# Performance work log

Measured on AMD Instinct MI355X. Metric: run time of the kernel, lower is better.

Reference implementation:

```python
import jax, jax.numpy as jnp
import numpy as np

B, S, D, H = 2, 2048, 1024, 16
HD = D // H


def setup_inputs() -> dict:
    key = jax.random.key(0)
    ks = jax.random.split(key, 7)
    q = jax.random.normal(ks[0], (B, S, D), jnp.float32)
    k = jax.random.normal(ks[1], (B, S, D), jnp.float32)
    v = jax.random.normal(ks[2], (B, S, D), jnp.float32)
    attention_mask = jnp.ones((B, S), jnp.int32)  # padding mask, 1 = keep
    bound = float(np.sqrt(6.0 / (D + D)))  # xavier_uniform for square Linear
    Wq = jax.random.uniform(ks[3], (D, D), jnp.float32, -bound, bound)
    Wk = jax.random.uniform(ks[4], (D, D), jnp.float32, -bound, bound)
    Wv = jax.random.uniform(ks[5], (D, D), jnp.float32, -bound, bound)
    Wo = jax.random.uniform(ks[6], (D, D), jnp.float32, -bound, bound)
    return {"q": q, "k": k, "v": v, "attention_mask": attention_mask,
            "Wq": Wq, "Wk": Wk, "Wv": Wv, "Wo": Wo}


def reference(q, k, v, attention_mask, Wq, Wk, Wv, Wo):
    # nn.Linear (bias=False): y = x @ W.T ; then split heads [B,H,S,HD]
    def heads(x, W):
        return (x @ W.T).reshape(B, S, H, HD).transpose(0, 2, 1, 3)

    qh, kh, vh = heads(q, Wq), heads(k, Wk), heads(v, Wv)
    scale = 1.0 / jnp.sqrt(jnp.float32(HD))
    # causal additive mask (0 on/below diagonal, -inf above); adding before the
    # scale matches the original since -inf * scale == -inf
    causal = jnp.where(jnp.tril(jnp.ones((S, S), dtype=bool)), 0.0, -jnp.inf)
    attn = (jnp.einsum('bhld,bhsd->bhls', qh, kh) + causal) * scale  # [B,H,L,S]
    pad = attention_mask[:, None, None, :]  # [B,1,1,S] padding mask
    attn = jnp.where(pad == 0, -jnp.inf, attn)
    attn = jax.nn.softmax(attn, axis=-1)
    out = jnp.einsum('bhls,bhsd->bhld', attn, vh)
    out = out.transpose(0, 2, 1, 3).reshape(B, S, D)
    return out @ Wo.T
```

## Files before the change

kernel.cpp:

```cpp
#include <hip/hip_runtime.h>
#include <hip/hip_bf16.h>
#include <stdint.h>

#define DEV_INLINE __device__ __forceinline__

typedef unsigned short u16;
typedef __attribute__((ext_vector_type(8))) __bf16 bf16x8;
typedef __attribute__((ext_vector_type(4))) float f32x4;

constexpr int Bc = 2, Sc = 2048, Dc = 1024, Hc = 16, HDc = 64;
constexpr int Kdim = 1024;
constexpr size_t SEG4M = 4194304;
constexpr size_t SEG1M = 1048576;

DEV_INLINE u16 f32_to_bf16(float f) {
    unsigned int u = __builtin_bit_cast(unsigned int, f);
    unsigned int r = (u + 0x7fffu + ((u >> 16) & 1u)) >> 16;
    return (u16)r;
}

DEV_INLINE uint32_t cvtpk_bf16(float lo, float hi) {
    uint32_t r;
    asm("v_cvt_pk_bf16_f32 %0, %1, %2" : "=v"(r) : "v"(lo), "v"(hi));
    return r;
}

DEV_INLINE f32x4 mfma16(bf16x8 a, bf16x8 b, f32x4 c) {
    return __builtin_amdgcn_mfma_f32_16x16x32_bf16(a, b, c, 0, 0, 0);
}

DEV_INLINE void gload_lds16(const u16* g, u16* lds) {
    __builtin_amdgcn_global_load_lds(
        (const __attribute__((address_space(1))) void*)g,
        (__attribute__((address_space(3))) void*)lds,
        16, 0, 0);
}

__global__ __launch_bounds__(256) void cvt_all_kernel(
        const float* __restrict__ q, const float* __restrict__ k,
        const float* __restrict__ v, const float* __restrict__ wq,
        const float* __restrict__ wk, const float* __restrict__ wv,
        const float* __restrict__ wo, u16* __restrict__ dst) {
    int b = blockIdx.x;
    const float* src; size_t doff; int lb;
    if (b < 2048)      { src = q;  lb = b;        doff = 0; }
    else if (b < 4096) { src = k;  lb = b - 2048; doff = SEG4M; }
    else if (b < 6144) { src = v;  lb = b - 4096; doff = 2 * SEG4M; }
    else if (b < 6656) { src = wq; lb = b - 6144; doff = 3 * SEG4M; }
    else if (b < 7168) { src = wk; lb = b - 6656; doff = 3 * SEG4M + SEG1M; }
    else if (b < 7680) { src = wv; lb = b - 7168; doff = 3 * SEG4M + 2 * SEG1M; }
    else               { src = wo; lb = b - 7680; doff = 3 * SEG4M + 3 * SEG1M; }
    size_t i = ((size_t)lb * 256 + threadIdx.x) * 8;
    float4 a = *reinterpret_cast<const float4*>(src + i);
    float4 c = *reinterpret_cast<const float4*>(src + i + 4);
    union { u16 u[8]; uint4 v4; } o;
    o.u[0] = f32_to_bf16(a.x); o.u[1] = f32_to_bf16(a.y);
    o.u[2] = f32_to_bf16(a.z); o.u[3] = f32_to_bf16(a.w);
    o.u[4] = f32_to_bf16(c.x); o.u[5] = f32_to_bf16(c.y);
    o.u[6] = f32_to_bf16(c.z); o.u[7] = f32_to_bf16(c.w);
    *reinterpret_cast<uint4*>(dst + doff + i) = o.v4;
}

__global__ __launch_bounds__(256, 3) void gemm_qkv_kernel(
        const u16* __restrict__ Xb, const u16* __restrict__ Wb,
        u16* __restrict__ Ob) {
    __shared__ u16 Al[128 * 64];
    __shared__ u16 Bl[128 * 64];
    const int tid = threadIdx.x;
    const int l = tid & 63, w = tid >> 6;
    const int wm = w >> 1, wn = w & 1;
    const int l15 = l & 15, lg = l >> 4;
    const int lr = l >> 3, lc = (l & 7) * 8;

    int bid = blockIdx.x;
    int wid = (bid & 7) * 96 + (bid >> 3);
    int mt = wid / 24, nt = wid % 24;
    int seg = nt >> 3, ntl = nt & 7;

    const u16* A = Xb + (size_t)seg * SEG4M + (size_t)mt * 128 * Kdim;
    const u16* W = Wb + (size_t)seg * SEG1M + (size_t)ntl * 128 * Kdim;

    f32x4 acc[4][4] = {};

    for (int kt = 0; kt < 16; ++kt) {
        const int kb = kt * 64;
#pragma unroll
        for (int i = 0; i < 4; ++i) {
            int j = w * 4 + i;
            gload_lds16(A + (size_t)(j * 8 + lr) * Kdim + kb + lc, &Al[j * 512]);
            gload_lds16(W + (size_t)(j * 8 + lr) * Kdim + kb + lc, &Bl[j * 512]);
        }
        asm volatile("s_waitcnt vmcnt(0)" ::: "memory");
        __syncthreads();
#pragma unroll
        for (int kk = 0; kk < 2; ++kk) {
            bf16x8 af[4], bfr[4];
#pragma unroll
            for (int mi = 0; mi < 4; ++mi)
                af[mi] = *reinterpret_cast<const bf16x8*>(&Al[(wm * 64 + mi * 16 + l15) * 64 + kk * 32 + lg * 8]);
#pragma unroll
            for (int ni = 0; ni < 4; ++ni)
                bfr[ni] = *reinterpret_cast<const bf16x8*>(&Bl[(wn * 64 + ni * 16 + l15) * 64 + kk * 32 + lg * 8]);
#pragma unroll
            for (int mi = 0; mi < 4; ++mi)
#pragma unroll
                for (int ni = 0; ni < 4; ++ni)
                    acc[mi][ni] = mfma16(af[mi], bfr[ni], acc[mi][ni]);
        }
        __syncthreads();
    }

    const int row0 = mt * 128 + wm * 64;
    const int col0 = ntl * 128 + wn * 64;

    if (seg == 2) {
        u16* outT = Ob + 2 * SEG4M;
#pragma unroll
        for (int mi = 0; mi < 4; ++mi) {
            int m0 = row0 + mi * 16 + lg * 4;
            int b = m0 >> 11, s0 = m0 & 2047;
#pragma unroll
            for (int ni = 0; ni < 4; ++ni) {
                int n = col0 + ni * 16 + l15;
                int h = n >> 6, d = n & 63;
                int bh = b * Hc + h;
                uint2 pk;
                pk.x = ((uint32_t)f32_to_bf16(acc[mi][ni][1]) << 16) | f32_to_bf16(acc[mi][ni][0]);
                pk.y = ((uint32_t)f32_to_bf16(acc[mi][ni][3]) << 16) | f32_to_bf16(acc[mi][ni][2]);
                *reinterpret_cast<uint2*>(outT + ((size_t)bh * 64 + d) * Sc + s0) = pk;
            }
        }
    } else {
        const float scale = (seg == 0) ? 0.18033688f : 1.0f;
        u16* out = Ob + (size_t)seg * SEG4M;
#pragma unroll
        for (int mi = 0; mi < 4; ++mi)
#pragma unroll
            for (int r = 0; r < 4; ++r) {
                int m = row0 + mi * 16 + lg * 4 + r;
                int b = m >> 11, s = m & 2047;
#pragma unroll
                for (int ni = 0; ni < 4; ++ni) {
                    int n = col0 + ni * 16 + l15;
                    int h = n >> 6, d = n & 63;
                    out[(((size_t)b * Hc + h) * Sc + s) * HDc + d] =
                        f32_to_bf16(acc[mi][ni][r] * scale);
                }
            }
    }
}

__global__ __launch_bounds__(256, 3) void gemm_out_kernel(
        const u16* __restrict__ A0, const u16* __restrict__ W0,
        float* __restrict__ outf) {
    __shared__ u16 Al[128 * 64];
    __shared__ u16 Bl[64 * 64];
    const int tid = threadIdx.x;
    const int l = tid & 63, w = tid >> 6;
    const int l15 = l & 15, lg = l >> 4;
    const int lr = l >> 3, lc = (l & 7) * 8;

    int bid = blockIdx.x;
    int wid = (bid & 7) * 64 + (bid >> 3);
    int mt = wid >> 4, nt = wid & 15;

    const u16* A = A0 + (size_t)mt * 128 * Kdim;
    const u16* W = W0 + (size_t)nt * 64 * Kdim;

    f32x4 acc[2][4] = {};

    for (int kt = 0; kt < 16; ++kt) {
        const int kb = kt * 64;
#pragma unroll
        for (int i = 0; i < 4; ++i) {
            int j = w * 4 + i;
            gload_lds16(A + (size_t)(j * 8 + lr) * Kdim + kb + lc, &Al[j * 512]);
        }
#pragma unroll
        for (int i = 0; i < 2; ++i) {
            int j = w * 2 + i;
            gload_lds16(W + (size_t)(j * 8 + lr) * Kdim + kb + lc, &Bl[j * 512]);
        }
        asm volatile("s_waitcnt vmcnt(0)" ::: "memory");
        __syncthreads();
#pragma unroll
        for (int kk = 0; kk < 2; ++kk) {
            bf16x8 af[2], bfr[4];
#pragma unroll
            for (int mi = 0; mi < 2; ++mi)
                af[mi] = *reinterpret_cast<const bf16x8*>(&Al[(w * 32 + mi * 16 + l15) * 64 + kk * 32 + lg * 8]);
#pragma unroll
            for (int ni = 0; ni < 4; ++ni)
                bfr[ni] = *reinterpret_cast<const bf16x8*>(&Bl[(ni * 16 + l15) * 64 + kk * 32 + lg * 8]);
#pragma unroll
            for (int mi = 0; mi < 2; ++mi)
#pragma unroll
                for (int ni = 0; ni < 4; ++ni)
                    acc[mi][ni] = mfma16(af[mi], bfr[ni], acc[mi][ni]);
        }
        __syncthreads();
    }

#pragma unroll
    for (int mi = 0; mi < 2; ++mi)
#pragma unroll
        for (int r = 0; r < 4; ++r) {
            int m = mt * 128 + w * 32 + mi * 16 + lg * 4 + r;
#pragma unroll
            for (int ni = 0; ni < 4; ++ni) {
                int n = nt * 64 + ni * 16 + l15;
                outf[(size_t)m * 1024 + n] = acc[mi][ni][r];
            }
        }
}

__global__ __launch_bounds__(512, 4) void flash_attn_kernel(
        const u16* __restrict__ Qh, const u16* __restrict__ Kh,
        const u16* __restrict__ Vt, u16* __restrict__ Ctx) {
    __shared__ u16 Ksh[64][72];
    __shared__ u16 Vsh[64][72];
    __shared__ u16 Psh[8][16][72];

    const int tid = threadIdx.x;
    const int l = tid & 63, w = tid >> 6;
    const int l15 = l & 15, lg = l >> 4;

    const int bid = blockIdx.x;
    const int bh = bid & 31;
    const int qt = 15 - (bid >> 5);
    const int b = bh >> 4, h = bh & 15;
    const int qr0 = qt * 128 + w * 16;

    const u16* qb = Qh + ((size_t)bh * Sc + qr0) * 64;
    bf16x8 aq[2];
#pragma unroll
    for (int kk = 0; kk < 2; ++kk)
        aq[kk] = *reinterpret_cast<const bf16x8*>(
            qb + (size_t)l15 * 64 + kk * 32 + lg * 8);

    f32x4 o[4] = {};
    float m_run = -1e30f, l_run = 0.f;

    const u16* kb0 = Kh + (size_t)bh * Sc * 64;
    const u16* vb0 = Vt + (size_t)bh * 64 * Sc;
    const int nkt = 2 * qt + 2;
    const int kt_max_w = qr0 >> 6;

    uint4 rk, rv;
    auto load_kv = [&](int kt) {
        int r = tid >> 3, cc = (tid & 7) * 8;
        rk = *reinterpret_cast<const uint4*>(kb0 + ((size_t)kt * 64 + r) * 64 + cc);
        rv = *reinterpret_cast<const uint4*>(vb0 + (size_t)r * Sc + kt * 64 + cc);
    };
    auto store_kv = [&]() {
        int r = tid >> 3, cc = (tid & 7) * 8;
        *reinterpret_cast<uint4*>(&Ksh[r][cc]) = rk;
        *reinterpret_cast<uint4*>(&Vsh[r][cc]) = rv;
    };

    load_kv(0);
    for (int kt = 0; kt < nkt; ++kt) {
        store_kv();
        __syncthreads();
        if (kt + 1 < nkt) load_kv(kt + 1);

        if (kt <= kt_max_w) {
            f32x4 sc[4] = {};
#pragma unroll
            for (int kk = 0; kk < 2; ++kk) {
                bf16x8 kf[4];
#pragma unroll
                for (int nk = 0; nk < 4; ++nk)
                    kf[nk] = *reinterpret_cast<const bf16x8*>(&Ksh[nk * 16 + l15][kk * 32 + lg * 8]);
                __builtin_amdgcn_s_setprio(1);
#pragma unroll
                for (int nk = 0; nk < 4; ++nk)
                    sc[nk] = mfma16(kf[nk], aq[kk], sc[nk]);
                __builtin_amdgcn_s_setprio(0);
            }

            if (kt == kt_max_w) {
                const int kb = kt * 64 + lg * 4;
                const int qg = qr0 + l15;
#pragma unroll
                for (int nk = 0; nk < 4; ++nk)
#pragma unroll
                    for (int r = 0; r < 4; ++r)
                        if (kb + nk * 16 + r > qg) sc[nk][r] = -1e30f;
            }

            float pmax = -1e30f;
#pragma unroll
            for (int nk = 0; nk < 4; ++nk)
#pragma unroll
                for (int r = 0; r < 4; ++r) pmax = fmaxf(pmax, sc[nk][r]);
            pmax = fmaxf(pmax, __shfl_xor(pmax, 16));
            pmax = fmaxf(pmax, __shfl_xor(pmax, 32));
            if (pmax > m_run + 11.5f) {
                float alpha = exp2f(m_run - pmax);
                l_run *= alpha;
#pragma unroll
                for (int nd = 0; nd < 4; ++nd)
#pragma unroll
                    for (int r = 0; r < 4; ++r) o[nd][r] *= alpha;
                m_run = pmax;
            }
            float ssum = 0.f;
#pragma unroll
            for (int nk = 0; nk < 4; ++nk)
#pragma unroll
                for (int r = 0; r < 4; ++r) {
                    float p = exp2f(sc[nk][r] - m_run);
                    sc[nk][r] = p;
                    ssum += p;
                }
            ssum += __shfl_xor(ssum, 16);
            ssum += __shfl_xor(ssum, 32);
            l_run += ssum;
#pragma unroll
            for (int nk = 0; nk < 4; ++nk) {
                uint2 pk;
                pk.x = cvtpk_bf16(sc[nk][0], sc[nk][1]);
                pk.y = cvtpk_bf16(sc[nk][2], sc[nk][3]);
                *reinterpret_cast<uint2*>(&Psh[w][l15][nk * 16 + lg * 4]) = pk;
            }
            asm volatile("s_waitcnt lgkmcnt(0)" ::: "memory");
            __builtin_amdgcn_sched_barrier(0);

#pragma unroll
            for (int kk = 0; kk < 2; ++kk) {
                bf16x8 vf[4];
#pragma unroll
                for (int nd = 0; nd < 4; ++nd)
                    vf[nd] = *reinterpret_cast<const bf16x8*>(&Vsh[nd * 16 + l15][kk * 32 + lg * 8]);
                bf16x8 pa = *reinterpret_cast<const bf16x8*>(&Psh[w][l15][kk * 32 + lg * 8]);
                __builtin_amdgcn_s_setprio(1);
#pragma unroll
                for (int nd = 0; nd < 4; ++nd)
                    o[nd] = mfma16(vf[nd], pa, o[nd]);
                __builtin_amdgcn_s_setprio(0);
            }
        }
        __syncthreads();
    }

    {
        float inv = 1.f / l_run;
        int srow = qr0 + l15;
        size_t base = ((size_t)b * Sc + srow) * Dc + h * 64;
#pragma unroll
        for (int nd = 0; nd < 4; ++nd) {
            uint2 pk;
            pk.x = cvtpk_bf16(o[nd][0] * inv, o[nd][1] * inv);
            pk.y = cvtpk_bf16(o[nd][2] * inv, o[nd][3] * inv);
            *reinterpret_cast<uint2*>(Ctx + base + nd * 16 + lg * 4) = pk;
        }
    }
}

extern "C" void kernel_launch(void* const* d_in, const int* in_sizes, int n_in,
                              void* d_out, int out_size, void* d_ws, size_t ws_size,
                              hipStream_t stream) {
    const float* q  = (const float*)d_in[0];
    const float* k  = (const float*)d_in[1];
    const float* v  = (const float*)d_in[2];
    const float* Wq = (const float*)d_in[4];
    const float* Wk = (const float*)d_in[5];
    const float* Wv = (const float*)d_in[6];
    const float* Wo = (const float*)d_in[7];

    u16* ws = (u16*)d_ws;
    u16* Xq  = ws;
    u16* Wqb = ws + 3 * SEG4M;
    u16* Wob = Wqb + 3 * SEG1M;
    u16* Qh  = ws + 4 * SEG4M;
    u16* Kh  = Qh + SEG4M;
    u16* Vtr = Kh + SEG4M;
    u16* Ctx = ws;

    cvt_all_kernel<<<8192, 256, 0, stream>>>(q, k, v, Wq, Wk, Wv, Wo, ws);

    gemm_qkv_kernel<<<768, 256, 0, stream>>>(Xq, Wqb, Qh);

    flash_attn_kernel<<<512, 512, 0, stream>>>(Qh, Kh, Vtr, Ctx);

    gemm_out_kernel<<<512, 256, 0, stream>>>(Ctx, Wob, (float*)d_out);
}
```

Measured before the change: 123.9 us.

## Switch flash attention to 32x32x16 MFMA with register-resident P fragments

The attention kernel now has 4 waves per block, each covering 32 query rows, and uses 32x32x16 bf16 MFMAs instead of 16x16x32. The softmax probabilities are packed to bf16 and rearranged between half-waves with cross-lane shuffles, so they no longer round-trip through LDS. This removes the P shared buffer and its waitcnt barrier and cuts the row reductions to one shuffle step. In exchange each thread holds more accumulator registers and does more K/V staging loads, and the block shrinks to 256 threads, which changes occupancy.

```diff
diff --git a/kernel.cpp b/kernel.cpp
--- a/kernel.cpp
+++ b/kernel.cpp
@@ -7,6 +7,7 @@
 typedef unsigned short u16;
 typedef __attribute__((ext_vector_type(8))) __bf16 bf16x8;
 typedef __attribute__((ext_vector_type(4))) float f32x4;
+typedef __attribute__((ext_vector_type(16))) float f32x16;
 
 constexpr int Bc = 2, Sc = 2048, Dc = 1024, Hc = 16, HDc = 64;
 constexpr int Kdim = 1024;
@@ -27,6 +28,9 @@
 
 DEV_INLINE f32x4 mfma16(bf16x8 a, bf16x8 b, f32x4 c) {
     return __builtin_amdgcn_mfma_f32_16x16x32_bf16(a, b, c, 0, 0, 0);
+}
+DEV_INLINE f32x16 mfma32(bf16x8 a, bf16x8 b, f32x16 c) {
+    return __builtin_amdgcn_mfma_f32_32x32x16_bf16(a, b, c, 0, 0, 0);
 }
 
 DEV_INLINE void gload_lds16(const u16* g, u16* lds) {
@@ -214,31 +218,31 @@
         }
 }
 
-__global__ __launch_bounds__(512, 4) void flash_attn_kernel(
+__global__ __launch_bounds__(256, 2) void flash_attn_kernel(
         const u16* __restrict__ Qh, const u16* __restrict__ Kh,
         const u16* __restrict__ Vt, u16* __restrict__ Ctx) {
     __shared__ u16 Ksh[64][72];
     __shared__ u16 Vsh[64][72];
-    __shared__ u16 Psh[8][16][72];
 
     const int tid = threadIdx.x;
     const int l = tid & 63, w = tid >> 6;
-    const int l15 = l & 15, lg = l >> 4;
+    const int l31 = l & 31;
+    const int h = l >> 5;
 
     const int bid = blockIdx.x;
     const int bh = bid & 31;
     const int qt = 15 - (bid >> 5);
-    const int b = bh >> 4, h = bh & 15;
-    const int qr0 = qt * 128 + w * 16;
-
-    const u16* qb = Qh + ((size_t)bh * Sc + qr0) * 64;
-    bf16x8 aq[2];
-#pragma unroll
-    for (int kk = 0; kk < 2; ++kk)
-        aq[kk] = *reinterpret_cast<const bf16x8*>(
-            qb + (size_t)l15 * 64 + kk * 32 + lg * 8);
-
-    f32x4 o[4] = {};
+    const int b = bh >> 4, hh = bh & 15;
+    const int qr0 = qt * 128 + w * 32;
+    const int q = qr0 + l31;
+
+    const u16* qb = Qh + ((size_t)bh * Sc + q) * 64;
+    bf16x8 aq[4];
+#pragma unroll
+    for (int s = 0; s < 4; ++s)
+        aq[s] = *reinterpret_cast<const bf16x8*>(qb + s * 16 + h * 8);
+
+    f32x16 o[2] = {};
     float m_run = -1e30f, l_run = 0.f;
 
     const u16* kb0 = Kh + (size_t)bh * Sc * 64;
@@ -252,92 +256,113 @@
         rk = *reinterpret_cast<const uint4*>(kb0 + ((size_t)kt * 64 + r) * 64 + cc);
         rv = *reinterpret_cast<const uint4*>(vb0 + (size_t)r * Sc + kt * 64 + cc);
     };
+    uint4 rk2, rv2;
+    auto load_kv2 = [&](int kt) {
+        int r = 32 + (tid >> 3), cc = (tid & 7) * 8;
+        rk2 = *reinterpret_cast<const uint4*>(kb0 + ((size_t)kt * 64 + r) * 64 + cc);
+        rv2 = *reinterpret_cast<const uint4*>(vb0 + (size_t)r * Sc + kt * 64 + cc);
+    };
     auto store_kv = [&]() {
         int r = tid >> 3, cc = (tid & 7) * 8;
         *reinterpret_cast<uint4*>(&Ksh[r][cc]) = rk;
         *reinterpret_cast<uint4*>(&Vsh[r][cc]) = rv;
+        *reinterpret_cast<uint4*>(&Ksh[32 + r][cc]) = rk2;
+        *reinterpret_cast<uint4*>(&Vsh[32 + r][cc]) = rv2;
     };
 
-    load_kv(0);
+    load_kv(0); load_kv2(0);
     for (int kt = 0; kt < nkt; ++kt) {
         store_kv();
         __syncthreads();
-        if (kt + 1 < nkt) load_kv(kt + 1);
+        if (kt + 1 < nkt) { load_kv(kt + 1); load_kv2(kt + 1); }
 
         if (kt <= kt_max_w) {
-            f32x4 sc[4] = {};
-#pragma unroll
-            for (int kk = 0; kk < 2; ++kk) {
-                bf16x8 kf[4];
-#pragma unroll
-                for (int nk = 0; nk < 4; ++nk)
-                    kf[nk] = *reinterpret_cast<const bf16x8*>(&Ksh[nk * 16 + l15][kk * 32 + lg * 8]);
+            f32x16 sc[2] = {};
+#pragma unroll
+            for (int s = 0; s < 4; ++s) {
+                bf16x8 kf0 = *reinterpret_cast<const bf16x8*>(&Ksh[l31][s * 16 + h * 8]);
+                bf16x8 kf1 = *reinterpret_cast<const bf16x8*>(&Ksh[32 + l31][s * 16 + h * 8]);
                 __builtin_amdgcn_s_setprio(1);
-#pragma unroll
-                for (int nk = 0; nk < 4; ++nk)
-                    sc[nk] = mfma16(kf[nk], aq[kk], sc[nk]);
+                sc[0] = mfma32(kf0, aq[s], sc[0]);
+                sc[1] = mfma32(kf1, aq[s], sc[1]);
                 __builtin_amdgcn_s_setprio(0);
             }
 
             if (kt == kt_max_w) {
-                const int kb = kt * 64 + lg * 4;
-                const int qg = qr0 + l15;
-#pragma unroll
-                for (int nk = 0; nk < 4; ++nk)
-#pragma unroll
-                    for (int r = 0; r < 4; ++r)
-                        if (kb + nk * 16 + r > qg) sc[nk][r] = -1e30f;
+#pragma unroll
+                for (int nk = 0; nk < 2; ++nk)
+#pragma unroll
+                    for (int r = 0; r < 16; ++r) {
+                        int kpos = kt * 64 + nk * 32 + (r & 3) + 8 * (r >> 2) + 4 * h;
+                        if (kpos > q) sc[nk][r] = -1e30f;
+                    }
             }
 
             float pmax = -1e30f;
 #pragma unroll
-            for (int nk = 0; nk < 4; ++nk)
-#pragma unroll
-                for (int r = 0; r < 4; ++r) pmax = fmaxf(pmax, sc[nk][r]);
-            pmax = fmaxf(pmax, __shfl_xor(pmax, 16));
+            for (int nk = 0; nk < 2; ++nk)
+#pragma unroll
+                for (int r = 0; r < 16; ++r) pmax = fmaxf(pmax, sc[nk][r]);
             pmax = fmaxf(pmax, __shfl_xor(pmax, 32));
             if (pmax > m_run + 11.5f) {
                 float alpha = exp2f(m_run - pmax);
                 l_run *= alpha;
 #pragma unroll
-                for (int nd = 0; nd < 4; ++nd)
-#pragma unroll
-                    for (int r = 0; r < 4; ++r) o[nd][r] *= alpha;
+                for (int nd = 0; nd < 2; ++nd)
+#pragma unroll
+                    for (int r = 0; r < 16; ++r) o[nd][r] *= alpha;
                 m_run = pmax;
             }
             float ssum = 0.f;
 #pragma unroll
-            for (int nk = 0; nk < 4; ++nk)
-#pragma unroll
-                for (int r = 0; r < 4; ++r) {
+            for (int nk = 0; nk < 2; ++nk)
+#pragma unroll
+                for (int r = 0; r < 16; ++r) {
                     float p = exp2f(sc[nk][r] - m_run);
                     sc[nk][r] = p;
                     ssum += p;
                 }
-            ssum += __shfl_xor(ssum, 16);
             ssum += __shfl_xor(ssum, 32);
             l_run += ssum;
-#pragma unroll
-            for (int nk = 0; nk < 4; ++nk) {
-                uint2 pk;
-                pk.x = cvtpk_bf16(sc[nk][0], sc[nk][1]);
-                pk.y = cvtpk_bf16(sc[nk][2], sc[nk][3]);
-                *reinterpret_cast<uint2*>(&Psh[w][l15][nk * 16 + lg * 4]) = pk;
-            }
-            asm volatile("s_waitcnt lgkmcnt(0)" ::: "memory");
-            __builtin_amdgcn_sched_barrier(0);
-
-#pragma unroll
-            for (int kk = 0; kk < 2; ++kk) {
-                bf16x8 vf[4];
-#pragma unroll
-                for (int nd = 0; nd < 4; ++nd)
-                    vf[nd] = *reinterpret_cast<const bf16x8*>(&Vsh[nd * 16 + l15][kk * 32 + lg * 8]);
-                bf16x8 pa = *reinterpret_cast<const bf16x8*>(&Psh[w][l15][kk * 32 + lg * 8]);
+
+            uint32_t pk0[8], pk1[8];
+#pragma unroll
+            for (int t = 0; t < 8; ++t) {
+                pk0[t] = cvtpk_bf16(sc[0][2 * t], sc[0][2 * t + 1]);
+                pk1[t] = cvtpk_bf16(sc[1][2 * t], sc[1][2 * t + 1]);
+            }
+            uint32_t px0[8], px1[8];
+#pragma unroll
+            for (int t = 0; t < 8; ++t) {
+                px0[t] = __shfl_xor(pk0[t], 32);
+                px1[t] = __shfl_xor(pk1[t], 32);
+            }
+            union fragu { uint32_t d[4]; bf16x8 v; };
+            fragu fr[4];
+            fr[0].d[0] = h ? px0[2] : pk0[0];
+            fr[0].d[1] = h ? px0[3] : pk0[1];
+            fr[0].d[2] = h ? pk0[2] : px0[0];
+            fr[0].d[3] = h ? pk0[3] : px0[1];
+            fr[1].d[0] = h ? px0[6] : pk0[4];
+            fr[1].d[1] = h ? px0[7] : pk0[5];
+            fr[1].d[2] = h ? pk0[6] : px0[4];
+            fr[1].d[3] = h ? pk0[7] : px0[5];
+            fr[2].d[0] = h ? px1[2] : pk1[0];
+            fr[2].d[1] = h ? px1[3] : pk1[1];
+            fr[2].d[2] = h ? pk1[2] : px1[0];
+            fr[2].d[3] = h ? pk1[3] : px1[1];
+            fr[3].d[0] = h ? px1[6] : pk1[4];
+            fr[3].d[1] = h ? px1[7] : pk1[5];
+            fr[3].d[2] = h ? pk1[6] : px1[4];
+            fr[3].d[3] = h ? pk1[7] : px1[5];
+
+#pragma unroll
+            for (int s = 0; s < 4; ++s) {
+                bf16x8 vf0 = *reinterpret_cast<const bf16x8*>(&Vsh[l31][s * 16 + h * 8]);
+                bf16x8 vf1 = *reinterpret_cast<const bf16x8*>(&Vsh[32 + l31][s * 16 + h * 8]);
                 __builtin_amdgcn_s_setprio(1);
-#pragma unroll
-                for (int nd = 0; nd < 4; ++nd)
-                    o[nd] = mfma16(vf[nd], pa, o[nd]);
+                o[0] = mfma32(vf0, fr[s].v, o[0]);
+                o[1] = mfma32(vf1, fr[s].v, o[1]);
                 __builtin_amdgcn_s_setprio(0);
             }
         }
@@ -346,15 +371,17 @@
 
     {
         float inv = 1.f / l_run;
-        int srow = qr0 + l15;
-        size_t base = ((size_t)b * Sc + srow) * Dc + h * 64;
-#pragma unroll
-        for (int nd = 0; nd < 4; ++nd) {
-            uint2 pk;
-            pk.x = cvtpk_bf16(o[nd][0] * inv, o[nd][1] * inv);
-            pk.y = cvtpk_bf16(o[nd][2] * inv, o[nd][3] * inv);
-            *reinterpret_cast<uint2*>(Ctx + base + nd * 16 + lg * 4) = pk;
-        }
+        size_t base = ((size_t)b * Sc + q) * Dc + hh * 64;
+#pragma unroll
+        for (int nd = 0; nd < 2; ++nd)
+#pragma unroll
+            for (int g = 0; g < 4; ++g) {
+                int d0 = nd * 32 + g * 8 + h * 4;
+                uint2 pkt;
+                pkt.x = cvtpk_bf16(o[nd][4 * g] * inv, o[nd][4 * g + 1] * inv);
+                pkt.y = cvtpk_bf16(o[nd][4 * g + 2] * inv, o[nd][4 * g + 3] * inv);
+                *reinterpret_cast<uint2*>(Ctx + base + d0) = pkt;
+            }
     }
 }
 
@@ -382,7 +409,7 @@
 
     gemm_qkv_kernel<<<768, 256, 0, stream>>>(Xq, Wqb, Qh);
 
-    flash_attn_kernel<<<512, 512, 0, stream>>>(Qh, Kh, Vtr, Ctx);
+    flash_attn_kernel<<<512, 256, 0, stream>>>(Qh, Kh, Vtr, Ctx);
 
     gemm_out_kernel<<<512, 256, 0, stream>>>(Ctx, Wob, (float*)d_out);
 }
```

New measurement: 123.8 us. Within noise of the previous version (-0.1%).
